# Optimization experiments

Measured on AMD Instinct MI355X. Metric: run time of the kernel, lower is better.

The kernel has to match this reference:

```python
import jax, jax.numpy as jnp
import numpy as np

N_NODES = 50000
DIM_IN, DIM_H, DIM_OUT = 128, 128, 64


def gcn_conv(x, src, dst, W, b):
    """PyG GCNConv: D^{-1/2}(A+I)D^{-1/2} X W + b, self-loops handled analytically."""
    N = x.shape[0]
    h = x @ W  # [N, dout]
    # in-degree on dst plus 1 for the self loop (PyG computes deg on col/dst)
    deg = jnp.zeros((N,), dtype=x.dtype).at[dst].add(1.0) + 1.0
    dinv = jax.lax.rsqrt(deg)  # deg >= 1 thanks to self loop
    norm = dinv[src] * dinv[dst]  # [E]
    agg = jax.ops.segment_sum(h[src] * norm[:, None], dst, num_segments=N)
    agg = agg + h * (dinv * dinv)[:, None]  # self-loop term: dinv_i^2 * h_i
    return agg + b


def setup_inputs() -> dict:
    key = jax.random.key(0)
    k1, k2, k3, k4, k5 = jax.random.split(key, 5)
    x = jax.random.normal(k1, (N_NODES, DIM_IN), dtype=jnp.float32)
    edge_index = jax.random.randint(k2, (2, 600000), 0, N_NODES, dtype=jnp.int64)
    # Glorot-ish init for weights, zero bias (as in torch defaults for GCNConv)
    W1 = jax.random.normal(k3, (DIM_IN, DIM_H), dtype=jnp.float32) / np.sqrt(DIM_IN)
    b1 = jnp.zeros((DIM_H,), dtype=jnp.float32)
    W2 = jax.random.normal(k4, (DIM_H, DIM_OUT), dtype=jnp.float32) / np.sqrt(DIM_H)
    b2 = jnp.zeros((DIM_OUT,), dtype=jnp.float32)
    return {"x": x, "edge_index": edge_index, "W1": W1, "b1": b1, "W2": W2, "b2": b2}


def reference(x, edge_index, W1, b1, W2, b2):
    src, dst = edge_index[0], edge_index[1]
    h = gcn_conv(x, src, dst, W1, b1)
    h = jax.nn.relu(h)
    h = gcn_conv(h, src, dst, W2, b2)
    return jax.nn.log_softmax(h, axis=1)
```

## Files before the change

kernel.cpp:

```cpp
#include <hip/hip_runtime.h>


typedef short bf16x8 __attribute__((ext_vector_type(8)));
typedef float f32x4 __attribute__((ext_vector_type(4)));
typedef unsigned u32x4 __attribute__((ext_vector_type(4)));

static constexpr int CAP = 64;

static __device__ __forceinline__ short f2bf(float f) {
  union { float f; unsigned u; } v; v.f = f;
  unsigned r = v.u + 0x7fff + ((v.u >> 16) & 1);
  return (short)(r >> 16);
}
static __device__ __forceinline__ float bf2f(unsigned u16) {
  union { unsigned u; float f; } v; v.u = u16 << 16; return v.f;
}
static __device__ __forceinline__ float dinv_of(int cur, int node) {
  return rsqrtf((float)(cur - (node << 6) + 1));
}


__global__ __launch_bounds__(256) void k_init(const float* __restrict__ W1,
                                              const float* __restrict__ W2,
                                              unsigned short* __restrict__ WT1,
                                              unsigned short* __restrict__ WT2,
                                              int* __restrict__ cursor, int n) {
  int t = blockIdx.x * 256 + threadIdx.x;
  if (t < n) cursor[t] = t << 6;
  if (t < 128 * 128) {
    int k = t >> 7, nn = t & 127;
    WT1[nn * 128 + k] = (unsigned short)f2bf(W1[t]);
  }
  if (t < 128 * 64) {
    int k = t >> 6, nn = t & 63;
    WT2[nn * 128 + k] = (unsigned short)f2bf(W2[t]);
  }
}


__global__ __launch_bounds__(256) void k_fill(const int* __restrict__ src,
                                              const int* __restrict__ dst,
                                              int* __restrict__ cursor,
                                              unsigned short* __restrict__ col,
                                              int E) {
  int t = blockIdx.x * 256 + threadIdx.x;
  int E4 = E >> 2;
  if (t < E4) {
    int4 d = ((const int4*)dst)[t];
    int4 s = ((const int4*)src)[t];
    int p0 = atomicAdd(&cursor[d.x], 1);
    int p1 = atomicAdd(&cursor[d.y], 1);
    int p2 = atomicAdd(&cursor[d.z], 1);
    int p3 = atomicAdd(&cursor[d.w], 1);
    if (p0 < (d.x << 6) + CAP) col[p0] = (unsigned short)s.x;
    if (p1 < (d.y << 6) + CAP) col[p1] = (unsigned short)s.y;
    if (p2 < (d.z << 6) + CAP) col[p2] = (unsigned short)s.z;
    if (p3 < (d.w << 6) + CAP) col[p3] = (unsigned short)s.w;
  }
  if (t == 0) {
    for (int e = E4 << 2; e < E; ++e) {
      int d = dst[e];
      int pos = atomicAdd(&cursor[d], 1);
      if (pos < (d << 6) + CAP) col[pos] = (unsigned short)src[e];
    }
  }
}

template <int BN, bool ABF16>
static __device__ __forceinline__ void gemm_body(
    int bid, int tid, const void* __restrict__ Xv,
    const unsigned short* __restrict__ WT, const int* __restrict__ cursor,
    unsigned short* __restrict__ Hout, int n, unsigned char* WL) {
  constexpr int NT = BN / 16;
  constexpr int PITCH = 272;
  {
    const float4* srcw = (const float4*)WT;
#pragma unroll 4
    for (int q = tid; q < BN * 16; q += 256) {
      int r = q >> 4, c = q & 15;
      *(float4*)(&WL[r * PITCH + c * 16]) = srcw[q];
    }
  }
  __syncthreads();

  int wave = tid >> 6, lane = tid & 63;
  int lr = lane & 15, lg = lane >> 4;
  int row = bid * 64 + wave * 16 + lr;
  int arow = (row < n) ? row : (n - 1);

  bf16x8 af[4];
  if (ABF16) {
    const unsigned short* xr = (const unsigned short*)Xv + (size_t)arow * 128 + lg * 8;
#pragma unroll
    for (int t = 0; t < 4; ++t) af[t] = *(const bf16x8*)(xr + t * 32);
  } else {
    const float* xr = (const float*)Xv + (size_t)arow * 128 + lg * 8;
#pragma unroll
    for (int t = 0; t < 4; ++t) {
      float4 lo = *(const float4*)(xr + t * 32);
      float4 hi = *(const float4*)(xr + t * 32 + 4);
      bf16x8 a;
      a[0] = f2bf(lo.x); a[1] = f2bf(lo.y); a[2] = f2bf(lo.z); a[3] = f2bf(lo.w);
      a[4] = f2bf(hi.x); a[5] = f2bf(hi.y); a[6] = f2bf(hi.z); a[7] = f2bf(hi.w);
      af[t] = a;
    }
  }

  f32x4 acc[NT];
#pragma unroll
  for (int j = 0; j < NT; ++j) acc[j] = (f32x4){0.f, 0.f, 0.f, 0.f};

#pragma unroll
  for (int j = 0; j < NT; ++j) {
    const unsigned char* bp = &WL[(size_t)(j * 16 + lr) * PITCH + lg * 16];
#pragma unroll
    for (int t = 0; t < 4; ++t) {
      bf16x8 bfr = *(const bf16x8*)(bp + t * 64);
      acc[j] = __builtin_amdgcn_mfma_f32_16x16x32_bf16(af[t], bfr, acc[j], 0, 0, 0);
    }
  }

  int crow0 = bid * 64 + wave * 16 + lg * 4;
#pragma unroll
  for (int r = 0; r < 4; ++r) {
    int gr = crow0 + r;
    if (gr < n) {
      float sc = dinv_of(cursor[gr], gr);
#pragma unroll
      for (int j = 0; j < NT; ++j)
        Hout[(size_t)gr * BN + j * 16 + lr] = (unsigned short)f2bf(acc[j][r] * sc);
    }
  }
}

__global__ __launch_bounds__(256) void k_gemm1(const float* __restrict__ X,
                                               const unsigned short* __restrict__ WT,
                                               const int* __restrict__ cursor,
                                               unsigned short* __restrict__ Hout, int n) {
  __shared__ unsigned char WL[128 * 272];
  gemm_body<128, false>(blockIdx.x, threadIdx.x, X, WT, cursor, Hout, n, WL);
}

__global__ __launch_bounds__(256) void k_gemm2(const unsigned short* __restrict__ X,
                                               const unsigned short* __restrict__ WT,
                                               const int* __restrict__ cursor,
                                               unsigned short* __restrict__ Hout, int n) {
  __shared__ unsigned char WL[64 * 272];
  gemm_body<64, true>(blockIdx.x, threadIdx.x, X, WT, cursor, Hout, n, WL);
}


__global__ __launch_bounds__(256) void k_gather128(const int* __restrict__ cursor,
                                                   const unsigned short* __restrict__ col,
                                                   const unsigned* __restrict__ H1,
                                                   const float* __restrict__ b,
                                                   unsigned* __restrict__ OUT, int n) {
  int tid = threadIdx.x;
  int lane = tid & 63;
  int g = lane >> 4, sub = lane & 15;
  int node = blockIdx.x * 16 + (tid >> 6) * 4 + g;
  if (node >= n) return;
  int e0 = node << 6;
  int cur = cursor[node];
  float di = dinv_of(cur, node);
  int e1 = min(cur, e0 + CAP);
  const u32x4* H4 = (const u32x4*)H1;
  float acc[8];
#pragma unroll
  for (int j = 0; j < 8; ++j) acc[j] = 0.f;
  int e = e0;
  for (; e + 4 <= e1; e += 4) {
    u32x4 v0 = H4[(size_t)col[e] * 16 + sub];
    u32x4 v1 = H4[(size_t)col[e + 1] * 16 + sub];
    u32x4 v2 = H4[(size_t)col[e + 2] * 16 + sub];
    u32x4 v3 = H4[(size_t)col[e + 3] * 16 + sub];
#pragma unroll
    for (int j = 0; j < 4; ++j) {
      acc[2 * j]     += (bf2f(v0[j] & 0xffff) + bf2f(v1[j] & 0xffff)) +
                        (bf2f(v2[j] & 0xffff) + bf2f(v3[j] & 0xffff));
      acc[2 * j + 1] += (bf2f(v0[j] >> 16) + bf2f(v1[j] >> 16)) +
                        (bf2f(v2[j] >> 16) + bf2f(v3[j] >> 16));
    }
  }
  for (; e < e1; ++e) {
    u32x4 v0 = H4[(size_t)col[e] * 16 + sub];
#pragma unroll
    for (int j = 0; j < 4; ++j) {
      acc[2 * j]     += bf2f(v0[j] & 0xffff);
      acc[2 * j + 1] += bf2f(v0[j] >> 16);
    }
  }
  u32x4 vs = H4[(size_t)node * 16 + sub];
  float4 b0 = *(const float4*)(b + 8 * sub);
  float4 b1 = *(const float4*)(b + 8 * sub + 4);
  float bb[8] = {b0.x, b0.y, b0.z, b0.w, b1.x, b1.y, b1.z, b1.w};
  u32x4 o;
#pragma unroll
  for (int j = 0; j < 4; ++j) {
    float vx = fmaxf((acc[2 * j] + bf2f(vs[j] & 0xffff)) * di + bb[2 * j], 0.f);
    float vy = fmaxf((acc[2 * j + 1] + bf2f(vs[j] >> 16)) * di + bb[2 * j + 1], 0.f);
    o[j] = (unsigned)(unsigned short)f2bf(vx) |
           ((unsigned)(unsigned short)f2bf(vy) << 16);
  }
  ((u32x4*)OUT)[(size_t)node * 16 + sub] = o;
}

__global__ __launch_bounds__(256) void k_gather64_lsm(const int* __restrict__ cursor,
                                                      const unsigned short* __restrict__ col,
                                                      const unsigned* __restrict__ H2,
                                                      const float* __restrict__ b,
                                                      float* __restrict__ OUT, int n) {
  int tid = threadIdx.x;
  int lane = tid & 63;
  int g = lane >> 3, sub = lane & 7;
  int node = blockIdx.x * 32 + (tid >> 6) * 8 + g;
  if (node >= n) return;
  int e0 = node << 6;
  int cur = cursor[node];
  float di = dinv_of(cur, node);
  int e1 = min(cur, e0 + CAP);
  const u32x4* H4 = (const u32x4*)H2;
  float acc[8];
#pragma unroll
  for (int j = 0; j < 8; ++j) acc[j] = 0.f;
  int e = e0;
  for (; e + 4 <= e1; e += 4) {
    u32x4 v0 = H4[(size_t)col[e] * 8 + sub];
    u32x4 v1 = H4[(size_t)col[e + 1] * 8 + sub];
    u32x4 v2 = H4[(size_t)col[e + 2] * 8 + sub];
    u32x4 v3 = H4[(size_t)col[e + 3] * 8 + sub];
#pragma unroll
    for (int j = 0; j < 4; ++j) {
      acc[2 * j]     += (bf2f(v0[j] & 0xffff) + bf2f(v1[j] & 0xffff)) +
                        (bf2f(v2[j] & 0xffff) + bf2f(v3[j] & 0xffff));
      acc[2 * j + 1] += (bf2f(v0[j] >> 16) + bf2f(v1[j] >> 16)) +
                        (bf2f(v2[j] >> 16) + bf2f(v3[j] >> 16));
    }
  }
  for (; e < e1; ++e) {
    u32x4 v0 = H4[(size_t)col[e] * 8 + sub];
#pragma unroll
    for (int j = 0; j < 4; ++j) {
      acc[2 * j]     += bf2f(v0[j] & 0xffff);
      acc[2 * j + 1] += bf2f(v0[j] >> 16);
    }
  }
  u32x4 vs = H4[(size_t)node * 8 + sub];
  float4 b0 = *(const float4*)(b + 8 * sub);
  float4 b1 = *(const float4*)(b + 8 * sub + 4);
  float bb[8] = {b0.x, b0.y, b0.z, b0.w, b1.x, b1.y, b1.z, b1.w};
  float v[8];
#pragma unroll
  for (int j = 0; j < 4; ++j) {
    v[2 * j]     = (acc[2 * j] + bf2f(vs[j] & 0xffff)) * di + bb[2 * j];
    v[2 * j + 1] = (acc[2 * j + 1] + bf2f(vs[j] >> 16)) * di + bb[2 * j + 1];
  }
  float m = v[0];
#pragma unroll
  for (int j = 1; j < 8; ++j) m = fmaxf(m, v[j]);
#pragma unroll
  for (int off = 1; off < 8; off <<= 1) m = fmaxf(m, __shfl_xor(m, off));
  float s = 0.f;
#pragma unroll
  for (int j = 0; j < 8; ++j) s += expf(v[j] - m);
#pragma unroll
  for (int off = 1; off < 8; off <<= 1) s += __shfl_xor(s, off);
  float ls = logf(s) + m;
  float4 o0 = make_float4(v[0] - ls, v[1] - ls, v[2] - ls, v[3] - ls);
  float4 o1 = make_float4(v[4] - ls, v[5] - ls, v[6] - ls, v[7] - ls);
  float* op = OUT + (size_t)node * 64 + 8 * sub;
  *(float4*)op = o0;
  *(float4*)(op + 4) = o1;
}


extern "C" void kernel_launch(void* const* d_in, const int* in_sizes, int n_in,
                              void* d_out, int out_size, void* d_ws, size_t ws_size,
                              hipStream_t stream) {
  const float* x  = (const float*)d_in[0];
  const int*   ei = (const int*)d_in[1];
  const float* W1 = (const float*)d_in[2];
  const float* b1 = (const float*)d_in[3];
  const float* W2 = (const float*)d_in[4];
  const float* b2 = (const float*)d_in[5];
  float* out = (float*)d_out;

  const int N = in_sizes[0] / 128;
  const int E = in_sizes[1] / 2;
  const int* src = ei;
  const int* dst = ei + E;
  const int NB = (N + 255) / 256;

  int*            cursor = (int*)d_ws;
  unsigned short* WT1    = (unsigned short*)(cursor + N);
  unsigned short* WT2    = WT1 + 128 * 128;
  unsigned short* col    = WT2 + 64 * 128;
  unsigned short* bufH1  = col + (size_t)N * CAP;
  unsigned short* bufR   = bufH1 + (size_t)N * 128;
  unsigned short* bufH2  = bufR + (size_t)N * 128;

  k_init<<<NB, 256, 0, stream>>>(W1, W2, WT1, WT2, cursor, N);
  k_fill<<<(E / 4 + 255) / 256, 256, 0, stream>>>(src, dst, cursor, col, E);

  const int gemm_grid = (N + 63) / 64;

  k_gemm1<<<gemm_grid, 256, 0, stream>>>(x, WT1, cursor, bufH1, N);
  k_gather128<<<(N + 15) / 16, 256, 0, stream>>>(cursor, col,
                                                 (const unsigned*)bufH1, b1,
                                                 (unsigned*)bufR, N);

  k_gemm2<<<gemm_grid, 256, 0, stream>>>(bufR, WT2, cursor, bufH2, N);
  k_gather64_lsm<<<(N + 31) / 32, 256, 0, stream>>>(cursor, col,
                                                    (const unsigned*)bufH2, b2,
                                                    out, N);
}
```

Measured before the change: 110.2 us.

## Fuse layer-1 gather with layer-2 GEMM into single kernel

Merges the 128-wide neighbor aggregation (bias, ReLU) with the second GEMM, so each lane aggregates a full row's slice and feeds it straight into MFMA fragments. This removes the intermediate bufR write and read plus one kernel launch. In exchange, each lane now handles one node with four gathers per edge, so fewer lanes share each node's edge list and load balance across nodes with different degrees gets worse. W2 is also read directly from global memory instead of LDS.

```diff
diff --git a/kernel.cpp b/kernel.cpp
--- a/kernel.cpp
+++ b/kernel.cpp
@@ -66,13 +66,14 @@
   }
 }
 
-template <int BN, bool ABF16>
-static __device__ __forceinline__ void gemm_body(
-    int bid, int tid, const void* __restrict__ Xv,
-    const unsigned short* __restrict__ WT, const int* __restrict__ cursor,
-    unsigned short* __restrict__ Hout, int n, unsigned char* WL) {
-  constexpr int NT = BN / 16;
-  constexpr int PITCH = 272;
+__global__ __launch_bounds__(256) void k_gemm1(const float* __restrict__ X,
+                                               const unsigned short* __restrict__ WT,
+                                               const int* __restrict__ cursor,
+                                               unsigned short* __restrict__ Hout,
+                                               int n) {
+  constexpr int BN = 128, NT = BN / 16, PITCH = 272;
+  __shared__ unsigned char WL[BN * PITCH];
+  int tid = threadIdx.x;
   {
     const float4* srcw = (const float4*)WT;
 #pragma unroll 4
@@ -85,16 +86,12 @@
 
   int wave = tid >> 6, lane = tid & 63;
   int lr = lane & 15, lg = lane >> 4;
-  int row = bid * 64 + wave * 16 + lr;
+  int row = blockIdx.x * 64 + wave * 16 + lr;
   int arow = (row < n) ? row : (n - 1);
 
   bf16x8 af[4];
-  if (ABF16) {
-    const unsigned short* xr = (const unsigned short*)Xv + (size_t)arow * 128 + lg * 8;
-#pragma unroll
-    for (int t = 0; t < 4; ++t) af[t] = *(const bf16x8*)(xr + t * 32);
-  } else {
-    const float* xr = (const float*)Xv + (size_t)arow * 128 + lg * 8;
+  {
+    const float* xr = X + (size_t)arow * 128 + lg * 8;
 #pragma unroll
     for (int t = 0; t < 4; ++t) {
       float4 lo = *(const float4*)(xr + t * 32);
@@ -109,7 +106,6 @@
   f32x4 acc[NT];
 #pragma unroll
   for (int j = 0; j < NT; ++j) acc[j] = (f32x4){0.f, 0.f, 0.f, 0.f};
-
 #pragma unroll
   for (int j = 0; j < NT; ++j) {
     const unsigned char* bp = &WL[(size_t)(j * 16 + lr) * PITCH + lg * 16];
@@ -120,7 +116,7 @@
     }
   }
 
-  int crow0 = bid * 64 + wave * 16 + lg * 4;
+  int crow0 = blockIdx.x * 64 + wave * 16 + lg * 4;
 #pragma unroll
   for (int r = 0; r < 4; ++r) {
     int gr = crow0 + r;
@@ -133,76 +129,101 @@
   }
 }
 
-__global__ __launch_bounds__(256) void k_gemm1(const float* __restrict__ X,
-                                               const unsigned short* __restrict__ WT,
-                                               const int* __restrict__ cursor,
-                                               unsigned short* __restrict__ Hout, int n) {
-  __shared__ unsigned char WL[128 * 272];
-  gemm_body<128, false>(blockIdx.x, threadIdx.x, X, WT, cursor, Hout, n, WL);
-}
-
-__global__ __launch_bounds__(256) void k_gemm2(const unsigned short* __restrict__ X,
-                                               const unsigned short* __restrict__ WT,
-                                               const int* __restrict__ cursor,
-                                               unsigned short* __restrict__ Hout, int n) {
-  __shared__ unsigned char WL[64 * 272];
-  gemm_body<64, true>(blockIdx.x, threadIdx.x, X, WT, cursor, Hout, n, WL);
-}
-
-
-__global__ __launch_bounds__(256) void k_gather128(const int* __restrict__ cursor,
-                                                   const unsigned short* __restrict__ col,
-                                                   const unsigned* __restrict__ H1,
-                                                   const float* __restrict__ b,
-                                                   unsigned* __restrict__ OUT, int n) {
+__global__ __launch_bounds__(256) void k_g128_gemm2(
+    const int* __restrict__ cursor, const unsigned short* __restrict__ col,
+    const unsigned* __restrict__ H1, const float* __restrict__ b,
+    const unsigned short* __restrict__ WT, unsigned short* __restrict__ H2,
+    int n) {
   int tid = threadIdx.x;
-  int lane = tid & 63;
-  int g = lane >> 4, sub = lane & 15;
-  int node = blockIdx.x * 16 + (tid >> 6) * 4 + g;
-  if (node >= n) return;
-  int e0 = node << 6;
-  int cur = cursor[node];
-  float di = dinv_of(cur, node);
+  int lane = tid & 63, wave = tid >> 6;
+  int lr = lane & 15, lg = lane >> 4;
+  int node = blockIdx.x * 64 + wave * 16 + lr;
+  int nd = (node < n) ? node : (n - 1);
+  int e0 = nd << 6;
+  int cur = cursor[nd];
+  float di = dinv_of(cur, nd);
   int e1 = min(cur, e0 + CAP);
   const u32x4* H4 = (const u32x4*)H1;
-  float acc[8];
-#pragma unroll
-  for (int j = 0; j < 8; ++j) acc[j] = 0.f;
+
+  float acc[4][8];
+#pragma unroll
+  for (int t = 0; t < 4; ++t)
+#pragma unroll
+    for (int j = 0; j < 8; ++j) acc[t][j] = 0.f;
+
   int e = e0;
-  for (; e + 4 <= e1; e += 4) {
-    u32x4 v0 = H4[(size_t)col[e] * 16 + sub];
-    u32x4 v1 = H4[(size_t)col[e + 1] * 16 + sub];
-    u32x4 v2 = H4[(size_t)col[e + 2] * 16 + sub];
-    u32x4 v3 = H4[(size_t)col[e + 3] * 16 + sub];
+  for (; e + 2 <= e1; e += 2) {
+    int s0 = col[e], s1 = col[e + 1];
+    u32x4 va[4], vb[4];
+#pragma unroll
+    for (int t = 0; t < 4; ++t) {
+      va[t] = H4[(size_t)s0 * 16 + t * 4 + lg];
+      vb[t] = H4[(size_t)s1 * 16 + t * 4 + lg];
+    }
+#pragma unroll
+    for (int t = 0; t < 4; ++t)
+#pragma unroll
+      for (int j = 0; j < 4; ++j) {
+        acc[t][2 * j]     += bf2f(va[t][j] & 0xffff) + bf2f(vb[t][j] & 0xffff);
+        acc[t][2 * j + 1] += bf2f(va[t][j] >> 16) + bf2f(vb[t][j] >> 16);
+      }
+  }
+  for (; e < e1; ++e) {
+    int s0 = col[e];
+#pragma unroll
+    for (int t = 0; t < 4; ++t) {
+      u32x4 v = H4[(size_t)s0 * 16 + t * 4 + lg];
+#pragma unroll
+      for (int j = 0; j < 4; ++j) {
+        acc[t][2 * j]     += bf2f(v[j] & 0xffff);
+        acc[t][2 * j + 1] += bf2f(v[j] >> 16);
+      }
+    }
+  }
+
+  bf16x8 af[4];
+#pragma unroll
+  for (int t = 0; t < 4; ++t) {
+    u32x4 vs = H4[(size_t)nd * 16 + t * 4 + lg];
+    const float* bp = b + lg * 8 + t * 32;
+    float4 c0 = *(const float4*)bp;
+    float4 c1 = *(const float4*)(bp + 4);
+    float bb[8] = {c0.x, c0.y, c0.z, c0.w, c1.x, c1.y, c1.z, c1.w};
+    bf16x8 a;
 #pragma unroll
     for (int j = 0; j < 4; ++j) {
-      acc[2 * j]     += (bf2f(v0[j] & 0xffff) + bf2f(v1[j] & 0xffff)) +
-                        (bf2f(v2[j] & 0xffff) + bf2f(v3[j] & 0xffff));
-      acc[2 * j + 1] += (bf2f(v0[j] >> 16) + bf2f(v1[j] >> 16)) +
-                        (bf2f(v2[j] >> 16) + bf2f(v3[j] >> 16));
-    }
-  }
-  for (; e < e1; ++e) {
-    u32x4 v0 = H4[(size_t)col[e] * 16 + sub];
-#pragma unroll
-    for (int j = 0; j < 4; ++j) {
-      acc[2 * j]     += bf2f(v0[j] & 0xffff);
-      acc[2 * j + 1] += bf2f(v0[j] >> 16);
-    }
-  }
-  u32x4 vs = H4[(size_t)node * 16 + sub];
-  float4 b0 = *(const float4*)(b + 8 * sub);
-  float4 b1 = *(const float4*)(b + 8 * sub + 4);
-  float bb[8] = {b0.x, b0.y, b0.z, b0.w, b1.x, b1.y, b1.z, b1.w};
-  u32x4 o;
+      float vx = fmaxf((acc[t][2 * j] + bf2f(vs[j] & 0xffff)) * di + bb[2 * j], 0.f);
+      float vy = fmaxf((acc[t][2 * j + 1] + bf2f(vs[j] >> 16)) * di + bb[2 * j + 1], 0.f);
+      a[2 * j] = f2bf(vx);
+      a[2 * j + 1] = f2bf(vy);
+    }
+    af[t] = a;
+  }
+
+  f32x4 o[4];
+#pragma unroll
+  for (int j = 0; j < 4; ++j) o[j] = (f32x4){0.f, 0.f, 0.f, 0.f};
 #pragma unroll
   for (int j = 0; j < 4; ++j) {
-    float vx = fmaxf((acc[2 * j] + bf2f(vs[j] & 0xffff)) * di + bb[2 * j], 0.f);
-    float vy = fmaxf((acc[2 * j + 1] + bf2f(vs[j] >> 16)) * di + bb[2 * j + 1], 0.f);
-    o[j] = (unsigned)(unsigned short)f2bf(vx) |
-           ((unsigned)(unsigned short)f2bf(vy) << 16);
-  }
-  ((u32x4*)OUT)[(size_t)node * 16 + sub] = o;
+    const unsigned short* wp = WT + (size_t)(j * 16 + lr) * 128 + lg * 8;
+#pragma unroll
+    for (int t = 0; t < 4; ++t) {
+      bf16x8 bfr = *(const bf16x8*)(wp + t * 32);
+      o[j] = __builtin_amdgcn_mfma_f32_16x16x32_bf16(af[t], bfr, o[j], 0, 0, 0);
+    }
+  }
+
+  int crow0 = blockIdx.x * 64 + wave * 16 + lg * 4;
+#pragma unroll
+  for (int r = 0; r < 4; ++r) {
+    int gr = crow0 + r;
+    if (gr < n) {
+      float sc = dinv_of(cursor[gr], gr);
+#pragma unroll
+      for (int j = 0; j < 4; ++j)
+        H2[(size_t)gr * 64 + j * 16 + lr] = (unsigned short)f2bf(o[j][r] * sc);
+    }
+  }
 }
 
 __global__ __launch_bounds__(256) void k_gather64_lsm(const int* __restrict__ cursor,
@@ -296,8 +317,7 @@
   unsigned short* WT2    = WT1 + 128 * 128;
   unsigned short* col    = WT2 + 64 * 128;
   unsigned short* bufH1  = col + (size_t)N * CAP;
-  unsigned short* bufR   = bufH1 + (size_t)N * 128;
-  unsigned short* bufH2  = bufR + (size_t)N * 128;
+  unsigned short* bufH2  = bufH1 + (size_t)N * 128;
 
   k_init<<<NB, 256, 0, stream>>>(W1, W2, WT1, WT2, cursor, N);
   k_fill<<<(E / 4 + 255) / 256, 256, 0, stream>>>(src, dst, cursor, col, E);
@@ -305,11 +325,11 @@
   const int gemm_grid = (N + 63) / 64;
 
   k_gemm1<<<gemm_grid, 256, 0, stream>>>(x, WT1, cursor, bufH1, N);
-  k_gather128<<<(N + 15) / 16, 256, 0, stream>>>(cursor, col,
-                                                 (const unsigned*)bufH1, b1,
-                                                 (unsigned*)bufR, N);
-
-  k_gemm2<<<gemm_grid, 256, 0, stream>>>(bufR, WT2, cursor, bufH2, N);
+
+  k_g128_gemm2<<<gemm_grid, 256, 0, stream>>>(cursor, col,
+                                              (const unsigned*)bufH1, b1,
+                                              WT2, bufH2, N);
+
   k_gather64_lsm<<<(N + 31) / 32, 256, 0, stream>>>(cursor, col,
                                                     (const unsigned*)bufH2, b2,
                                                     out, N);
```

Result: slower. 119.4 us (+8.3%).
